# Kernel tuning notes

Hardware: AMD Instinct MI355X
Metric: run time of the kernel (lower is better)

Reference implementation:

```python
import jax, jax.numpy as jnp
import numpy as np

N_NODES = 50000
N_EDGES = 800000
N_REL = 8
OUT_CH = 64      # latent dim of z
HID = 128        # hidden_channels
IN_CH = 128      # reconstructed feature dim
NEG_SLOPE = 0.2


def rgat_conv(x, src, dst, edge_type, weight, q, k, bias, num_nodes):
    """PyG RGATConv, heads=1, dim=1, additive-self-attention, across-relation.
    x: [N, in]; weight: [R, in, out]; q,k: [out, 1]; bias: [out]."""
    # per-relation transform of all nodes, then per-edge gather (same math as
    # per-edge bmm with weight[edge_type], avoids [E, in, out] intermediate)
    x_all = jnp.einsum('ni,rio->nro', x, weight)          # [N, R, out]
    x_j = x_all[src, edge_type]                            # [E, out]
    x_i = x_all[dst, edge_type]                            # [E, out]
    alpha = (x_i @ q + x_j @ k)[:, 0]                      # [E]
    alpha = jax.nn.leaky_relu(alpha, NEG_SLOPE)
    # scatter-softmax over destination neighborhoods
    m = jax.ops.segment_max(alpha, dst, num_segments=num_nodes)
    m = jnp.where(jnp.isfinite(m), m, 0.0)                 # empty segments -> 0
    ex = jnp.exp(alpha - m[dst])
    denom = jax.ops.segment_sum(ex, dst, num_segments=num_nodes)
    a = ex / (denom[dst] + 1e-16)                          # [E]
    out = jax.ops.segment_sum(a[:, None] * x_j, dst, num_segments=num_nodes)
    return out + bias


def setup_inputs() -> dict:
    key = jax.random.key(0)
    ks = jax.random.split(key, 12)
    z = jax.random.normal(ks[0], (N_NODES, OUT_CH), dtype=jnp.float32)
    edge_index = jax.random.randint(ks[1], (2, N_EDGES), 0, N_NODES, dtype=jnp.int32)
    edge_type = jax.random.randint(ks[2], (N_EDGES,), 0, N_REL, dtype=jnp.int32)

    def glorot(k_, shape):
        fan = shape[-2] + shape[-1]
        return jax.random.normal(k_, shape, dtype=jnp.float32) * jnp.sqrt(2.0 / fan)

    return {
        'z': z,
        'lin_w': glorot(ks[3], (HID, OUT_CH)),
        'lin_b': jnp.zeros((HID,), dtype=jnp.float32),
        'w1': glorot(ks[4], (N_REL, HID, HID)),
        'q1': glorot(ks[5], (HID, 1)),
        'k1': glorot(ks[6], (HID, 1)),
        'b1': jnp.zeros((HID,), dtype=jnp.float32),
        'w2': glorot(ks[7], (N_REL, HID, IN_CH)),
        'q2': glorot(ks[8], (IN_CH, 1)),
        'k2': glorot(ks[9], (IN_CH, 1)),
        'b2': jnp.zeros((IN_CH,), dtype=jnp.float32),
        'edge_index': edge_index,
        'edge_type': edge_type,
    }


def reference(z, lin_w, lin_b, w1, q1, k1, b1, w2, q2, k2, b2, edge_index, edge_type):
    num_nodes = z.shape[0]
    src, dst = edge_index[0], edge_index[1]
    h = z @ lin_w.T + lin_b                                 # nn.Linear
    h = jax.nn.relu(rgat_conv(h, src, dst, edge_type, w1, q1, k1, b1, num_nodes))
    # dropout is identity in eval mode
    recon_x = rgat_conv(h, src, dst, edge_type, w2, q2, k2, b2, num_nodes)
    return recon_x
```

## Files before the change

kernel.cpp:

```cpp
#include <hip/hip_runtime.h>
#include <hip/hip_bf16.h>
#include <cstdint>
#include <cstddef>

#define N_NODES 50000
#define N_EDGES 800000
#define NSEG    (N_NODES * 8)

using frag_t = __attribute__((ext_vector_type(8))) short;
using f32x4  = __attribute__((ext_vector_type(4))) float;

typedef const __attribute__((address_space(1))) void* gptr_t;
typedef __attribute__((address_space(3))) void* lptr_t;

__device__ __forceinline__ short f2bf(float x) {
    __hip_bfloat16 h = __float2bfloat16(x);
    return *reinterpret_cast<short*>(&h);
}
__device__ __forceinline__ float bf2f(unsigned int u) {
    union { unsigned int i; float f; } v;
    v.i = u << 16;
    return v.f;
}
__device__ __forceinline__ unsigned int packbf2(float lo, float hi) {
    unsigned int a = (unsigned short)f2bf(lo);
    unsigned int b = (unsigned short)f2bf(hi);
    return a | (b << 16);
}


__global__ void hist_kernel(const int* __restrict__ dst, const int* __restrict__ et,
                            int* __restrict__ deg8, int E) {
    int e = blockIdx.x * 256 + threadIdx.x;
    if (e < E) atomicAdd(&deg8[dst[e] * 8 + et[e]], 1);
}

__global__ __launch_bounds__(256) void scan_part(const int* __restrict__ deg8,
                                                 int* __restrict__ part, int M) {
    __shared__ int red[256];
    int t = threadIdx.x;
    int idx = blockIdx.x * 1024 + t * 4;
    int s = 0;
    if (idx + 3 < M) {
        int4 d = *(const int4*)(deg8 + idx);
        s = d.x + d.y + d.z + d.w;
    } else {
        for (int c = 0; c < 4; c++) if (idx + c < M) s += deg8[idx + c];
    }
    red[t] = s;
    __syncthreads();
    #pragma unroll
    for (int off = 128; off; off >>= 1) {
        if (t < off) red[t] += red[t + off];
        __syncthreads();
    }
    if (t == 0) part[blockIdx.x] = red[0];
}

__global__ __launch_bounds__(512) void scan_mid(int* __restrict__ part, int nparts,
                                                int* __restrict__ rowp, int M) {
    __shared__ int buf[512];
    int t = threadIdx.x;
    int own = (t < nparts) ? part[t] : 0;
    buf[t] = own;
    __syncthreads();
    for (int off = 1; off < 512; off <<= 1) {
        int v = buf[t];
        int u = (t >= off) ? buf[t - off] : 0;
        __syncthreads();
        buf[t] = v + u;
        __syncthreads();
    }
    if (t < nparts) part[t] = buf[t] - own;
    if (t == 511) rowp[M] = buf[511];
}

__global__ __launch_bounds__(256) void scan_fix(const int* __restrict__ deg8,
                                                const int* __restrict__ part,
                                                int* __restrict__ rowp,
                                                int* __restrict__ cursor, int M) {
    __shared__ int wsum[4];
    int t = threadIdx.x, lane = t & 63, w = t >> 6;
    int idx = blockIdx.x * 1024 + t * 4;
    int v0 = 0, v1 = 0, v2 = 0, v3 = 0;
    if (idx + 3 < M) {
        int4 d = *(const int4*)(deg8 + idx);
        v0 = d.x; v1 = d.y; v2 = d.z; v3 = d.w;
    } else {
        if (idx     < M) v0 = deg8[idx];
        if (idx + 1 < M) v1 = deg8[idx + 1];
        if (idx + 2 < M) v2 = deg8[idx + 2];
        if (idx + 3 < M) v3 = deg8[idx + 3];
    }
    int tsum = v0 + v1 + v2 + v3;
    int sc = tsum;
    #pragma unroll
    for (int off = 1; off < 64; off <<= 1) {
        int u = __shfl_up(sc, off, 64);
        if (lane >= off) sc += u;
    }
    if (lane == 63) wsum[w] = sc;
    __syncthreads();
    int woff = 0;
    for (int i = 0; i < w; i++) woff += wsum[i];
    int excl = part[blockIdx.x] + woff + sc - tsum;
    if (idx     < M) { rowp[idx]     = excl; cursor[idx]     = excl; } excl += v0;
    if (idx + 1 < M) { rowp[idx + 1] = excl; cursor[idx + 1] = excl; } excl += v1;
    if (idx + 2 < M) { rowp[idx + 2] = excl; cursor[idx + 2] = excl; } excl += v2;
    if (idx + 3 < M) { rowp[idx + 3] = excl; cursor[idx + 3] = excl; }
}

__global__ void fill_kernel(const int* __restrict__ src, const int* __restrict__ dst,
                            const int* __restrict__ et, int* __restrict__ cursor,
                            int* __restrict__ sorted, int E) {
    int e = blockIdx.x * 256 + threadIdx.x;
    if (e < E) {
        int pos = atomicAdd(&cursor[dst[e] * 8 + et[e]], 1);
        sorted[pos] = src[e] | (et[e] << 16);
    }
}


__global__ __launch_bounds__(256) void gemm_lin(const float* __restrict__ A,
                                                const float* __restrict__ B,
                                                const float* __restrict__ bias,
                                                unsigned short* __restrict__ hb, int N) {
    const int Kdim = 64;
    __shared__ float As[32][64];
    __shared__ float Bs[32][128];
    int t = threadIdx.x;
    int n0 = blockIdx.x * 64;
    int rg = t >> 4, cg = t & 15;
    int an = t >> 2, ak = (t & 3) * 8;
    float acc[4][8] = {};

    for (int k0 = 0; k0 < Kdim; k0 += 32) {
        int gn = n0 + an;
        if (gn < N) {
            const float* ap = A + (size_t)gn * Kdim + k0 + ak;
            float4 v0 = *(const float4*)ap;
            float4 v1 = *(const float4*)(ap + 4);
            As[ak + 0][an] = v0.x; As[ak + 1][an] = v0.y;
            As[ak + 2][an] = v0.z; As[ak + 3][an] = v0.w;
            As[ak + 4][an] = v1.x; As[ak + 5][an] = v1.y;
            As[ak + 6][an] = v1.z; As[ak + 7][an] = v1.w;
        } else {
            #pragma unroll
            for (int c = 0; c < 8; c++) As[ak + c][an] = 0.f;
        }
        {
            int o = t >> 1, kh = (t & 1) * 16;
            const float* bp = B + (size_t)o * Kdim + k0 + kh;
            #pragma unroll
            for (int j = 0; j < 4; j++) {
                float4 v = ((const float4*)bp)[j];
                Bs[kh + j * 4 + 0][o] = v.x;
                Bs[kh + j * 4 + 1][o] = v.y;
                Bs[kh + j * 4 + 2][o] = v.z;
                Bs[kh + j * 4 + 3][o] = v.w;
            }
        }
        __syncthreads();
        #pragma unroll
        for (int k = 0; k < 32; k++) {
            float a[4], b[8];
            *(float4*)&a[0] = *(const float4*)&As[k][rg * 4];
            *(float4*)&b[0] = *(const float4*)&Bs[k][cg * 8];
            *(float4*)&b[4] = *(const float4*)&Bs[k][cg * 8 + 4];
            #pragma unroll
            for (int i = 0; i < 4; i++)
                #pragma unroll
                for (int j = 0; j < 8; j++)
                    acc[i][j] = fmaf(a[i], b[j], acc[i][j]);
        }
        __syncthreads();
    }
    #pragma unroll
    for (int i = 0; i < 4; i++) {
        int gn = n0 + rg * 4 + i;
        if (gn < N) {
            unsigned short us[8];
            #pragma unroll
            for (int j = 0; j < 8; j++)
                us[j] = (unsigned short)f2bf(acc[i][j] + bias[cg * 8 + j]);
            *(int4*)(hb + (size_t)gn * 128 + cg * 8) = *(int4*)&us[0];
        }
    }
}


__global__ void wprep_kernel(const float* __restrict__ W, const float* __restrict__ q,
                             const float* __restrict__ k, short* __restrict__ Bf,
                             float* __restrict__ wq, float* __restrict__ wk) {
    int g = blockIdx.x * 256 + threadIdx.x;
    if (g < 131072) {
        int kk = g >> 7, o = g & 127;
        float v = W[(size_t)kk * 128 + o];
        Bf[(((size_t)(kk >> 3) * 128) + o) * 8 + (kk & 7)] = f2bf(v);
        return;
    }
    int h = g - 131072;
    if (h < 2048) {
        int which = h >> 10;
        int r = (h >> 7) & 7;
        int i = h & 127;
        const float* vec = which ? k : q;
        const float* wrow = W + ((size_t)r * 128 + i) * 128;
        float acc = 0.f;
        #pragma unroll 4
        for (int o = 0; o < 128; o++) acc = fmaf(wrow[o], vec[o], acc);
        (which ? wk : wq)[r * 128 + i] = acc;
    }
}


__global__ __launch_bounds__(256) void qk_table_kernel(const unsigned short* __restrict__ xb,
                                                       const float* __restrict__ wq,
                                                       const float* __restrict__ wk,
                                                       float* __restrict__ Q,
                                                       float* __restrict__ K, int N) {
    int n = blockIdx.x * 256 + threadIdx.x;
    if (n >= N) return;
    const uint2* row = (const uint2*)(xb + (size_t)n * 128);
    float aq[8] = {}, ak[8] = {};
    for (int i = 0; i < 32; i++) {
        uint2 d = row[i];
        float x0 = bf2f(d.x & 0xFFFFu);
        float x1 = bf2f(d.x >> 16);
        float x2 = bf2f(d.y & 0xFFFFu);
        float x3 = bf2f(d.y >> 16);
        int c = i * 4;
        #pragma unroll
        for (int r = 0; r < 8; r++) {
            const float* wqr = wq + r * 128 + c;
            const float* wkr = wk + r * 128 + c;
            aq[r] = fmaf(x0, wqr[0], fmaf(x1, wqr[1], fmaf(x2, wqr[2], fmaf(x3, wqr[3], aq[r]))));
            ak[r] = fmaf(x0, wkr[0], fmaf(x1, wkr[1], fmaf(x2, wkr[2], fmaf(x3, wkr[3], ak[r]))));
        }
    }
    float4* qp = (float4*)(Q + (size_t)n * 8);
    qp[0] = *(float4*)&aq[0];
    qp[1] = *(float4*)&aq[4];
    float4* kp = (float4*)(K + (size_t)n * 8);
    kp[0] = *(float4*)&ak[0];
    kp[1] = *(float4*)&ak[4];
}


__global__ __launch_bounds__(512, 8) void fused_agg_gemm(
        const unsigned short* __restrict__ hb,
        const float* __restrict__ Q,
        const float* __restrict__ Kt,
        const int* __restrict__ rowp8,
        const int* __restrict__ sorted,
        const short* __restrict__ Bf,
        const float* __restrict__ bias,
        float* __restrict__ Cout,
        unsigned short* __restrict__ hbout,
        int N, int relu) {
    __shared__ short s_tile[16 * 1024];
    __shared__ uint2 stash[8][64];
    __shared__ int wcnt;
    unsigned int* sdw = (unsigned int*)s_tile;
    const unsigned int* hbu = (const unsigned int*)hb;

    int t = threadIdx.x;
    int w = t >> 6, lane = t & 63;
    int lhi = lane >> 4, llo = lane & 15;
    int n0 = blockIdx.x * 16;

    if (t == 0) wcnt = 0;
    __syncthreads();

    for (;;) {
        int row;
        if (lane == 0) row = atomicAdd(&wcnt, 1);
        row = __shfl(row, 0, 64);
        if (row >= 16) break;
        int n = n0 + row;
        float2 acc = {0.f, 0.f};
        int rcur = 0;
        auto flushw = [&](unsigned int val) {
            int kb = rcur * 16 + (lane >> 2);
            sdw[kb * 64 + ((row ^ (kb & 15)) * 4) + (lane & 3)] = val;
        };
        if (n >= N) {
            while (rcur < 8) { flushw(0u); rcur++; }
            continue;
        }
        int beg = rowp8[n * 8];
        int end = rowp8[n * 8 + 8];
        int deg = end - beg;
        if (deg == 0) {
            while (rcur < 8) { flushw(0u); rcur++; }
            continue;
        }

        if (deg <= 64) {
            int pk = 0;
            float a = -INFINITY;
            if (lane < deg) {
                pk = sorted[beg + lane];
                int srcn = pk & 0xFFFF, etj = pk >> 16;
                a = Q[(size_t)n * 8 + etj] + Kt[(size_t)srcn * 8 + etj];
                a = (a > 0.f) ? a : 0.2f * a;
            }
            float m = a;
            #pragma unroll
            for (int off = 32; off; off >>= 1) m = fmaxf(m, __shfl_xor(m, off, 64));
            float e = (lane < deg) ? __expf(a - m) : 0.f;
            float sum = e;
            #pragma unroll
            for (int off = 32; off; off >>= 1) sum += __shfl_xor(sum, off, 64);
            float wgt = e / (sum + 1e-16f);
            stash[w][lane] = make_uint2((unsigned int)pk, __float_as_uint(wgt));

            int j = 0;
            for (; j + 8 <= deg; j += 8) {
                uint2 ee[8]; unsigned int dd[8];
                #pragma unroll
                for (int i = 0; i < 8; i++) ee[i] = stash[w][j + i];
                #pragma unroll
                for (int i = 0; i < 8; i++)
                    dd[i] = hbu[(size_t)(ee[i].x & 0xFFFFu) * 64 + lane];
                #pragma unroll
                for (int i = 0; i < 8; i++) {
                    int e0 = (int)(ee[i].x >> 16);
                    float w0 = __uint_as_float(ee[i].y);
                    while (rcur < e0) { flushw(packbf2(acc.x, acc.y)); acc.x = acc.y = 0.f; rcur++; }
                    acc.x = fmaf(w0, bf2f(dd[i] & 0xFFFF), acc.x);
                    acc.y = fmaf(w0, bf2f(dd[i] >> 16),    acc.y);
                }
            }
            for (; j < deg; j++) {
                uint2 e1 = stash[w][j];
                unsigned int d0 = hbu[(size_t)(e1.x & 0xFFFFu) * 64 + lane];
                int e0 = (int)(e1.x >> 16);
                float w0 = __uint_as_float(e1.y);
                while (rcur < e0) { flushw(packbf2(acc.x, acc.y)); acc.x = acc.y = 0.f; rcur++; }
                acc.x = fmaf(w0, bf2f(d0 & 0xFFFF), acc.x);
                acc.y = fmaf(w0, bf2f(d0 >> 16),    acc.y);
            }
            while (rcur < 8) { flushw(packbf2(acc.x, acc.y)); acc.x = acc.y = 0.f; rcur++; }
        } else {
            auto logit = [&](int j) -> float {
                int pk2 = sorted[beg + j];
                int srcn = pk2 & 0xFFFF, etj = pk2 >> 16;
                float aa = Q[(size_t)n * 8 + etj] + Kt[(size_t)srcn * 8 + etj];
                return (aa > 0.f) ? aa : 0.2f * aa;
            };
            float m = -INFINITY;
            for (int j = lane; j < deg; j += 64) m = fmaxf(m, logit(j));
            #pragma unroll
            for (int off = 32; off; off >>= 1) m = fmaxf(m, __shfl_xor(m, off, 64));
            float sum = 0.f;
            for (int j = lane; j < deg; j += 64) sum += __expf(logit(j) - m);
            #pragma unroll
            for (int off = 32; off; off >>= 1) sum += __shfl_xor(sum, off, 64);
            float inv = 1.f / (sum + 1e-16f);

            for (int j0 = 0; j0 < deg; j0 += 64) {
                int cnt = min(64, deg - j0);
                if (lane < cnt) {
                    int pk = sorted[beg + j0 + lane];
                    int srcn = pk & 0xFFFF, etj = pk >> 16;
                    float aa = Q[(size_t)n * 8 + etj] + Kt[(size_t)srcn * 8 + etj];
                    aa = (aa > 0.f) ? aa : 0.2f * aa;
                    float wgt = __expf(aa - m) * inv;
                    stash[w][lane] = make_uint2((unsigned int)pk, __float_as_uint(wgt));
                }
                for (int j = 0; j < cnt; j++) {
                    uint2 e1 = stash[w][j];
                    unsigned int d0 = hbu[(size_t)(e1.x & 0xFFFFu) * 64 + lane];
                    int e0 = (int)(e1.x >> 16);
                    float w0 = __uint_as_float(e1.y);
                    while (rcur < e0) { flushw(packbf2(acc.x, acc.y)); acc.x = acc.y = 0.f; rcur++; }
                    acc.x = fmaf(w0, bf2f(d0 & 0xFFFF), acc.x);
                    acc.y = fmaf(w0, bf2f(d0 >> 16),    acc.y);
                }
            }
            while (rcur < 8) { flushw(packbf2(acc.x, acc.y)); acc.x = acc.y = 0.f; rcur++; }
        }
    }
    __syncthreads();

    int ctb = w;
    f32x4 acc0 = {};
    const char* BfB = (const char*)Bf;
    #pragma unroll 4
    for (int kq = 0; kq < 32; kq++) {
        int kb = kq * 4 + lhi;
        int d = kb * 64 + ((llo ^ (kb & 15)) * 4);
        frag_t a  = *(const frag_t*)(&sdw[d]);
        frag_t b0 = *(const frag_t*)(BfB + ((size_t)kb * 128 + ctb * 16 + llo) * 16);
        acc0 = __builtin_amdgcn_mfma_f32_16x16x32_bf16(a, b0, acc0, 0, 0, 0);
    }

    {
        int col = ctb * 16 + llo;
        float bv = bias[col];
        #pragma unroll
        for (int rg = 0; rg < 4; rg++) {
            int rown = n0 + lhi * 4 + rg;
            if (rown < N) {
                float v = acc0[rg] + bv;
                if (relu) v = fmaxf(v, 0.f);
                if (Cout)  Cout[(size_t)rown * 128 + col] = v;
                if (hbout) hbout[(size_t)rown * 128 + col] = (unsigned short)f2bf(v);
            }
        }
    }
}


extern "C" void kernel_launch(void* const* d_in, const int* in_sizes, int n_in,
                              void* d_out, int out_size, void* d_ws, size_t ws_size,
                              hipStream_t stream) {
    const float* z     = (const float*)d_in[0];
    const float* lin_w = (const float*)d_in[1];
    const float* lin_b = (const float*)d_in[2];
    const float* w1    = (const float*)d_in[3];
    const float* q1    = (const float*)d_in[4];
    const float* k1    = (const float*)d_in[5];
    const float* b1    = (const float*)d_in[6];
    const float* w2    = (const float*)d_in[7];
    const float* q2    = (const float*)d_in[8];
    const float* k2    = (const float*)d_in[9];
    const float* b2    = (const float*)d_in[10];
    const int*   ei    = (const int*)d_in[11];
    const int*   et    = (const int*)d_in[12];
    float* out = (float*)d_out;

    char* ws = (char*)d_ws;
    size_t off = 0;
    auto alloc = [&](size_t bytes) -> void* {
        void* p = ws + off;
        off += (bytes + 255) & ~(size_t)255;
        return p;
    };
    unsigned short* hb  = (unsigned short*)alloc((size_t)N_NODES * 128 * 2);
    unsigned short* hb2 = (unsigned short*)alloc((size_t)N_NODES * 128 * 2);
    float* Q     = (float*)alloc((size_t)N_NODES * 8 * 4);
    float* K     = (float*)alloc((size_t)N_NODES * 8 * 4);
    int* sorted  = (int*)alloc((size_t)N_EDGES * 4);
    int* deg8    = (int*)alloc((size_t)NSEG * 4);
    int* rowp8   = (int*)alloc((size_t)(NSEG + 1) * 4);
    int* cursor8 = (int*)alloc((size_t)NSEG * 4);
    int* part    = (int*)alloc(1024 * 4);
    float* wq    = (float*)alloc(8 * 128 * 4);
    float* wk    = (float*)alloc(8 * 128 * 4);
    short* Bf    = (short*)alloc((size_t)1024 * 128 * 2);

    const int* src = ei;
    const int* dst = ei + N_EDGES;

    const int M = NSEG;
    const int nparts = (M + 1023) / 1024;

    hipMemsetAsync(deg8, 0, (size_t)M * 4, stream);
    hist_kernel<<<(N_EDGES + 255) / 256, 256, 0, stream>>>(dst, et, deg8, N_EDGES);
    scan_part<<<nparts, 256, 0, stream>>>(deg8, part, M);
    scan_mid<<<1, 512, 0, stream>>>(part, nparts, rowp8, M);
    scan_fix<<<nparts, 256, 0, stream>>>(deg8, part, rowp8, cursor8, M);
    fill_kernel<<<(N_EDGES + 255) / 256, 256, 0, stream>>>(src, dst, et, cursor8, sorted, N_EDGES);

    gemm_lin<<<(N_NODES + 63) / 64, 256, 0, stream>>>(z, lin_w, lin_b, hb, N_NODES);

    int fgrid = (N_NODES + 15) / 16;
    int qgrid = (N_NODES + 255) / 256;
    int wgrid = (131072 + 2048) / 256;

    wprep_kernel<<<wgrid, 256, 0, stream>>>(w1, q1, k1, Bf, wq, wk);
    qk_table_kernel<<<qgrid, 256, 0, stream>>>(hb, wq, wk, Q, K, N_NODES);
    fused_agg_gemm<<<fgrid, 512, 0, stream>>>(hb, Q, K, rowp8, sorted, Bf, b1,
                                              (float*)nullptr, hb2, N_NODES, 1);

    wprep_kernel<<<wgrid, 256, 0, stream>>>(w2, q2, k2, Bf, wq, wk);
    qk_table_kernel<<<qgrid, 256, 0, stream>>>(hb2, wq, wk, Q, K, N_NODES);
    fused_agg_gemm<<<fgrid, 512, 0, stream>>>(hb2, Q, K, rowp8, sorted, Bf, b2,
                                              out, (unsigned short*)nullptr, N_NODES, 0);
}
```

Baseline: 377.1 us.

## Fuse CSR build into one cooperative kernel and merge both weight preps

Replaces the memset, histogram, three scan kernels and fill kernel with a single cooperative-launch kernel that uses grid-wide syncs between phases. The two per-layer weight-prep kernels are merged into one launch that writes separate buffers for each layer. The aim is to cut kernel launch count and inter-kernel gaps. In exchange, grid.sync barriers and a fixed 391-block grid limit parallelism for the atomic histogram and fill phases, and the cooperative launch requires every block to be resident at once.

```diff
diff --git a/kernel.cpp b/kernel.cpp
--- a/kernel.cpp
+++ b/kernel.cpp
@@ -1,11 +1,15 @@
 #include <hip/hip_runtime.h>
 #include <hip/hip_bf16.h>
+#include <hip/hip_cooperative_groups.h>
 #include <cstdint>
 #include <cstddef>
+
+namespace cg = cooperative_groups;
 
 #define N_NODES 50000
 #define N_EDGES 800000
 #define NSEG    (N_NODES * 8)
+#define CSR_BLOCKS 391
 
 using frag_t = __attribute__((ext_vector_type(8))) short;
 using f32x4  = __attribute__((ext_vector_type(4))) float;
@@ -29,92 +33,112 @@
 }
 
 
-__global__ void hist_kernel(const int* __restrict__ dst, const int* __restrict__ et,
-                            int* __restrict__ deg8, int E) {
-    int e = blockIdx.x * 256 + threadIdx.x;
-    if (e < E) atomicAdd(&deg8[dst[e] * 8 + et[e]], 1);
-}
-
-__global__ __launch_bounds__(256) void scan_part(const int* __restrict__ deg8,
-                                                 int* __restrict__ part, int M) {
+__global__ __launch_bounds__(256) void coop_csr(
+        const int* __restrict__ src, const int* __restrict__ dst,
+        const int* __restrict__ et,
+        int* __restrict__ deg8, int* __restrict__ part,
+        int* __restrict__ rowp, int* __restrict__ cursor,
+        int* __restrict__ sorted) {
+    cg::grid_group grid = cg::this_grid();
     __shared__ int red[256];
-    int t = threadIdx.x;
-    int idx = blockIdx.x * 1024 + t * 4;
-    int s = 0;
-    if (idx + 3 < M) {
-        int4 d = *(const int4*)(deg8 + idx);
-        s = d.x + d.y + d.z + d.w;
-    } else {
-        for (int c = 0; c < 4; c++) if (idx + c < M) s += deg8[idx + c];
-    }
-    red[t] = s;
-    __syncthreads();
-    #pragma unroll
-    for (int off = 128; off; off >>= 1) {
-        if (t < off) red[t] += red[t + off];
+    __shared__ int buf[512];
+    __shared__ int wsum[4];
+
+    const int t = threadIdx.x, b = blockIdx.x;
+    const int gtid = b * 256 + t, gsz = CSR_BLOCKS * 256;
+
+    for (int i = gtid; i < NSEG; i += gsz) deg8[i] = 0;
+    grid.sync();
+
+    for (int e = gtid; e < N_EDGES; e += gsz)
+        atomicAdd(&deg8[dst[e] * 8 + et[e]], 1);
+    grid.sync();
+
+    {
+        int idx = b * 1024 + t * 4;
+        int s = 0;
+        if (idx + 3 < NSEG) {
+            int4 d = *(const int4*)(deg8 + idx);
+            s = d.x + d.y + d.z + d.w;
+        } else {
+            for (int c = 0; c < 4; c++) if (idx + c < NSEG) s += deg8[idx + c];
+        }
+        red[t] = s;
         __syncthreads();
-    }
-    if (t == 0) part[blockIdx.x] = red[0];
-}
-
-__global__ __launch_bounds__(512) void scan_mid(int* __restrict__ part, int nparts,
-                                                int* __restrict__ rowp, int M) {
-    __shared__ int buf[512];
-    int t = threadIdx.x;
-    int own = (t < nparts) ? part[t] : 0;
-    buf[t] = own;
-    __syncthreads();
-    for (int off = 1; off < 512; off <<= 1) {
-        int v = buf[t];
-        int u = (t >= off) ? buf[t - off] : 0;
+        #pragma unroll
+        for (int off = 128; off; off >>= 1) {
+            if (t < off) red[t] += red[t + off];
+            __syncthreads();
+        }
+        if (t == 0) part[b] = red[0];
+    }
+    grid.sync();
+
+    if (b == 0) {
+        buf[t]       = (t       < CSR_BLOCKS) ? part[t]       : 0;
+        buf[t + 256] = (t + 256 < CSR_BLOCKS) ? part[t + 256] : 0;
+        int offset = 1;
+        for (int d = 256; d > 0; d >>= 1) {
+            __syncthreads();
+            if (t < d) {
+                int ai = offset * (2 * t + 1) - 1;
+                int bi = offset * (2 * t + 2) - 1;
+                buf[bi] += buf[ai];
+            }
+            offset <<= 1;
+        }
         __syncthreads();
-        buf[t] = v + u;
+        if (t == 0) { rowp[NSEG] = buf[511]; buf[511] = 0; }
+        for (int d = 1; d < 512; d <<= 1) {
+            offset >>= 1;
+            __syncthreads();
+            if (t < d) {
+                int ai = offset * (2 * t + 1) - 1;
+                int bi = offset * (2 * t + 2) - 1;
+                int tv = buf[ai];
+                buf[ai] = buf[bi];
+                buf[bi] += tv;
+            }
+        }
         __syncthreads();
-    }
-    if (t < nparts) part[t] = buf[t] - own;
-    if (t == 511) rowp[M] = buf[511];
-}
-
-__global__ __launch_bounds__(256) void scan_fix(const int* __restrict__ deg8,
-                                                const int* __restrict__ part,
-                                                int* __restrict__ rowp,
-                                                int* __restrict__ cursor, int M) {
-    __shared__ int wsum[4];
-    int t = threadIdx.x, lane = t & 63, w = t >> 6;
-    int idx = blockIdx.x * 1024 + t * 4;
-    int v0 = 0, v1 = 0, v2 = 0, v3 = 0;
-    if (idx + 3 < M) {
-        int4 d = *(const int4*)(deg8 + idx);
-        v0 = d.x; v1 = d.y; v2 = d.z; v3 = d.w;
-    } else {
-        if (idx     < M) v0 = deg8[idx];
-        if (idx + 1 < M) v1 = deg8[idx + 1];
-        if (idx + 2 < M) v2 = deg8[idx + 2];
-        if (idx + 3 < M) v3 = deg8[idx + 3];
-    }
-    int tsum = v0 + v1 + v2 + v3;
-    int sc = tsum;
-    #pragma unroll
-    for (int off = 1; off < 64; off <<= 1) {
-        int u = __shfl_up(sc, off, 64);
-        if (lane >= off) sc += u;
-    }
-    if (lane == 63) wsum[w] = sc;
-    __syncthreads();
-    int woff = 0;
-    for (int i = 0; i < w; i++) woff += wsum[i];
-    int excl = part[blockIdx.x] + woff + sc - tsum;
-    if (idx     < M) { rowp[idx]     = excl; cursor[idx]     = excl; } excl += v0;
-    if (idx + 1 < M) { rowp[idx + 1] = excl; cursor[idx + 1] = excl; } excl += v1;
-    if (idx + 2 < M) { rowp[idx + 2] = excl; cursor[idx + 2] = excl; } excl += v2;
-    if (idx + 3 < M) { rowp[idx + 3] = excl; cursor[idx + 3] = excl; }
-}
-
-__global__ void fill_kernel(const int* __restrict__ src, const int* __restrict__ dst,
-                            const int* __restrict__ et, int* __restrict__ cursor,
-                            int* __restrict__ sorted, int E) {
-    int e = blockIdx.x * 256 + threadIdx.x;
-    if (e < E) {
+        if (t       < CSR_BLOCKS) part[t]       = buf[t];
+        if (t + 256 < CSR_BLOCKS) part[t + 256] = buf[t + 256];
+    }
+    grid.sync();
+
+    {
+        int lane = t & 63, w = t >> 6;
+        int idx = b * 1024 + t * 4;
+        int v0 = 0, v1 = 0, v2 = 0, v3 = 0;
+        if (idx + 3 < NSEG) {
+            int4 d = *(const int4*)(deg8 + idx);
+            v0 = d.x; v1 = d.y; v2 = d.z; v3 = d.w;
+        } else {
+            if (idx     < NSEG) v0 = deg8[idx];
+            if (idx + 1 < NSEG) v1 = deg8[idx + 1];
+            if (idx + 2 < NSEG) v2 = deg8[idx + 2];
+            if (idx + 3 < NSEG) v3 = deg8[idx + 3];
+        }
+        int tsum = v0 + v1 + v2 + v3;
+        int sc = tsum;
+        #pragma unroll
+        for (int off = 1; off < 64; off <<= 1) {
+            int u = __shfl_up(sc, off, 64);
+            if (lane >= off) sc += u;
+        }
+        if (lane == 63) wsum[w] = sc;
+        __syncthreads();
+        int woff = 0;
+        for (int i = 0; i < w; i++) woff += wsum[i];
+        int excl = part[b] + woff + sc - tsum;
+        if (idx     < NSEG) { rowp[idx]     = excl; cursor[idx]     = excl; } excl += v0;
+        if (idx + 1 < NSEG) { rowp[idx + 1] = excl; cursor[idx + 1] = excl; } excl += v1;
+        if (idx + 2 < NSEG) { rowp[idx + 2] = excl; cursor[idx + 2] = excl; } excl += v2;
+        if (idx + 3 < NSEG) { rowp[idx + 3] = excl; cursor[idx + 3] = excl; }
+    }
+    grid.sync();
+
+    for (int e = gtid; e < N_EDGES; e += gsz) {
         int pos = atomicAdd(&cursor[dst[e] * 8 + et[e]], 1);
         sorted[pos] = src[e] | (et[e] << 16);
     }
@@ -189,10 +213,23 @@
 }
 
 
-__global__ void wprep_kernel(const float* __restrict__ W, const float* __restrict__ q,
-                             const float* __restrict__ k, short* __restrict__ Bf,
-                             float* __restrict__ wq, float* __restrict__ wk) {
-    int g = blockIdx.x * 256 + threadIdx.x;
+__global__ void wprep2_kernel(const float* __restrict__ W1, const float* __restrict__ q1v,
+                              const float* __restrict__ k1v,
+                              const float* __restrict__ W2, const float* __restrict__ q2v,
+                              const float* __restrict__ k2v,
+                              short* __restrict__ Bf1, short* __restrict__ Bf2,
+                              float* __restrict__ wq1, float* __restrict__ wk1,
+                              float* __restrict__ wq2, float* __restrict__ wk2) {
+    int g0 = blockIdx.x * 256 + threadIdx.x;
+    int layer = (g0 >= 133120) ? 1 : 0;
+    int g = g0 - layer * 133120;
+    const float* W  = layer ? W2  : W1;
+    const float* qv = layer ? q2v : q1v;
+    const float* kv = layer ? k2v : k1v;
+    short* Bf = layer ? Bf2 : Bf1;
+    float* wq = layer ? wq2 : wq1;
+    float* wk = layer ? wk2 : wk1;
+
     if (g < 131072) {
         int kk = g >> 7, o = g & 127;
         float v = W[(size_t)kk * 128 + o];
@@ -204,7 +241,7 @@
         int which = h >> 10;
         int r = (h >> 7) & 7;
         int i = h & 127;
-        const float* vec = which ? k : q;
+        const float* vec = which ? kv : qv;
         const float* wrow = W + ((size_t)r * 128 + i) * 128;
         float acc = 0.f;
         #pragma unroll 4
@@ -447,36 +484,40 @@
     int* rowp8   = (int*)alloc((size_t)(NSEG + 1) * 4);
     int* cursor8 = (int*)alloc((size_t)NSEG * 4);
     int* part    = (int*)alloc(1024 * 4);
-    float* wq    = (float*)alloc(8 * 128 * 4);
-    float* wk    = (float*)alloc(8 * 128 * 4);
-    short* Bf    = (short*)alloc((size_t)1024 * 128 * 2);
+    float* wq1   = (float*)alloc(8 * 128 * 4);
+    float* wk1   = (float*)alloc(8 * 128 * 4);
+    float* wq2   = (float*)alloc(8 * 128 * 4);
+    float* wk2   = (float*)alloc(8 * 128 * 4);
+    short* Bf1   = (short*)alloc((size_t)1024 * 128 * 2);
+    short* Bf2   = (short*)alloc((size_t)1024 * 128 * 2);
 
     const int* src = ei;
     const int* dst = ei + N_EDGES;
 
-    const int M = NSEG;
-    const int nparts = (M + 1023) / 1024;
-
-    hipMemsetAsync(deg8, 0, (size_t)M * 4, stream);
-    hist_kernel<<<(N_EDGES + 255) / 256, 256, 0, stream>>>(dst, et, deg8, N_EDGES);
-    scan_part<<<nparts, 256, 0, stream>>>(deg8, part, M);
-    scan_mid<<<1, 512, 0, stream>>>(part, nparts, rowp8, M);
-    scan_fix<<<nparts, 256, 0, stream>>>(deg8, part, rowp8, cursor8, M);
-    fill_kernel<<<(N_EDGES + 255) / 256, 256, 0, stream>>>(src, dst, et, cursor8, sorted, N_EDGES);
+    {
+        const int* srcv = src; const int* dstv = dst; const int* etv = et;
+        int* deg8v = deg8; int* partv = part; int* rowpv = rowp8;
+        int* cursv = cursor8; int* sortv = sorted;
+        void* cargs[] = { (void*)&srcv, (void*)&dstv, (void*)&etv,
+                          (void*)&deg8v, (void*)&partv, (void*)&rowpv,
+                          (void*)&cursv, (void*)&sortv };
+        hipLaunchCooperativeKernel((const void*)coop_csr, dim3(CSR_BLOCKS), dim3(256),
+                                   cargs, 0, stream);
+    }
 
     gemm_lin<<<(N_NODES + 63) / 64, 256, 0, stream>>>(z, lin_w, lin_b, hb, N_NODES);
+
+    wprep2_kernel<<<(2 * 133120 + 255) / 256, 256, 0, stream>>>(
+        w1, q1, k1, w2, q2, k2, Bf1, Bf2, wq1, wk1, wq2, wk2);
 
     int fgrid = (N_NODES + 15) / 16;
     int qgrid = (N_NODES + 255) / 256;
-    int wgrid = (131072 + 2048) / 256;
-
-    wprep_kernel<<<wgrid, 256, 0, stream>>>(w1, q1, k1, Bf, wq, wk);
-    qk_table_kernel<<<qgrid, 256, 0, stream>>>(hb, wq, wk, Q, K, N_NODES);
-    fused_agg_gemm<<<fgrid, 512, 0, stream>>>(hb, Q, K, rowp8, sorted, Bf, b1,
+
+    qk_table_kernel<<<qgrid, 256, 0, stream>>>(hb, wq1, wk1, Q, K, N_NODES);
+    fused_agg_gemm<<<fgrid, 512, 0, stream>>>(hb, Q, K, rowp8, sorted, Bf1, b1,
                                               (float*)nullptr, hb2, N_NODES, 1);
 
-    wprep_kernel<<<wgrid, 256, 0, stream>>>(w2, q2, k2, Bf, wq, wk);
-    qk_table_kernel<<<qgrid, 256, 0, stream>>>(hb2, wq, wk, Q, K, N_NODES);
-    fused_agg_gemm<<<fgrid, 512, 0, stream>>>(hb2, Q, K, rowp8, sorted, Bf, b2,
+    qk_table_kernel<<<qgrid, 256, 0, stream>>>(hb2, wq2, wk2, Q, K, N_NODES);
+    fused_agg_gemm<<<fgrid, 512, 0, stream>>>(hb2, Q, K, rowp8, sorted, Bf2, b2,
                                               out, (unsigned short*)nullptr, N_NODES, 0);
 }
```

After: 614.6 us. +63.0%, slower.
